# Performance work log

Measured on AMD Instinct MI355X. Metric: run time of the kernel, lower is better.

The kernel has to match this reference:

```python
import jax, jax.numpy as jnp
import numpy as np

BATCH, SEQ, D_MODEL = 4, 4096, 2048
DSTATE, N_HEADS = 64, 16
D_INNER = DSTATE * N_HEADS  # 1024, must equal d_mamba


def setup_inputs() -> dict:
    key = jax.random.key(0)
    ks = jax.random.split(key, 6)
    x_norm = jax.random.normal(ks[0], (BATCH, SEQ, D_MODEL), jnp.float32)
    inv = 1.0 / np.sqrt(D_MODEL)
    Wx = jax.random.normal(ks[1], (D_INNER, D_MODEL), jnp.float32) * inv
    # dt_proj: weight std 0.001, bias -4.0 (as in module init)
    Wdt = jax.random.normal(ks[2], (D_INNER, D_MODEL), jnp.float32) * 0.001
    b_dt = jnp.full((D_INNER,), -4.0, jnp.float32)
    WB = jax.random.normal(ks[3], (DSTATE, D_MODEL), jnp.float32) * inv
    WC = jax.random.normal(ks[4], (DSTATE, D_MODEL), jnp.float32) * inv
    A_log = jnp.tile(jnp.log(jnp.arange(1, DSTATE + 1, dtype=jnp.float32))[None, :], (N_HEADS, 1))
    Dp = jnp.ones((D_INNER,), jnp.float32)
    Wout = jax.random.normal(ks[5], (D_INNER, D_INNER), jnp.float32) * (1.0 / np.sqrt(D_INNER))
    return {"x_norm": x_norm, "Wx": Wx, "Wdt": Wdt, "b_dt": b_dt,
            "WB": WB, "WC": WC, "A_log": A_log, "Dp": Dp, "Wout": Wout}


def reference(x_norm, Wx, Wdt, b_dt, WB, WC, A_log, Dp, Wout):
    # projections
    x_ssm = jnp.einsum("btd,id->bti", x_norm, Wx)                       # (B,T,D_inner)
    dt = jax.nn.softplus(jnp.einsum("btd,id->bti", x_norm, Wdt) + b_dt)
    dt = jnp.clip(dt, 1e-4, 0.5)
    Bm = jnp.einsum("btd,nd->btn", x_norm, WB)                          # (B,T,N)
    Cm = jnp.einsum("btd,nd->btn", x_norm, WC)
    Bm = Bm / jnp.maximum(jnp.linalg.norm(Bm, axis=-1, keepdims=True), 1.0)
    Cm = Cm / jnp.maximum(jnp.linalg.norm(Cm, axis=-1, keepdims=True), 1.0)
    # discretized diagonal SSM: h_t = dA_t * h_{t-1} + dt_t * B_t * x_t
    A_neg = -jnp.exp(A_log.reshape(-1))                                  # (D_inner,)
    dA = jnp.exp(dt * A_neg)                                             # (B,T,D_inner)
    B_exp = jnp.tile(Bm, (1, 1, N_HEADS))                                # repeat across heads
    C_exp = jnp.tile(Cm, (1, 1, N_HEADS))
    dBx = dt * B_exp * x_ssm

    def combine(c1, c2):
        a1, b1 = c1
        a2, b2 = c2
        return a2 * a1, a2 * b1 + b2

    _, h = jax.lax.associative_scan(combine, (dA, dBx), axis=1)          # (B,T,D_inner)
    y = C_exp * h + Dp * x_ssm
    return jnp.einsum("bti,oi->bto", y, Wout)
```

## Files before the change

### kernel.cpp

```cpp
#include <hip/hip_runtime.h>
#include <hip/hip_bf16.h>
#include <math.h>

#define BATCH  4
#define SEQ    4096
#define DMODEL 2048
#define DSTATE 64
#define DINNER 1024
#define MTOT   (BATCH*SEQ)
#define NPROJ  (DINNER+DINNER+DSTATE+DSTATE)
#define CH     128
#define NC     (SEQ/CH)

typedef __attribute__((ext_vector_type(8))) short bf16x8;
typedef __attribute__((ext_vector_type(4))) float f32x4;

__device__ __forceinline__ unsigned short f2bf(float v) {
    __hip_bfloat16 b = __float2bfloat16(v);
    unsigned short u; __builtin_memcpy(&u, &b, 2); return u;
}
__device__ __forceinline__ float bf2f(unsigned short u) {
    __hip_bfloat16 b; __builtin_memcpy(&b, &u, 2); return __bfloat162float(b);
}
__device__ __forceinline__ void split2(float v, unsigned short& h, unsigned short& l) {
    h = f2bf(v);
    l = f2bf(v - bf2f(h));
}

__global__ __launch_bounds__(256, 2)
void proj_gemm(const float* __restrict__ X,
               const unsigned short* __restrict__ Wh,
               const unsigned short* __restrict__ Wl,
               const float* __restrict__ b_dt,
               float* __restrict__ x_ssm, float* __restrict__ dt,
               float* __restrict__ Bm,    float* __restrict__ Cm)
{
    __shared__ unsigned short Ahs[128*32];
    __shared__ unsigned short Als[128*32];
    __shared__ unsigned short Bhs[128*32];
    __shared__ unsigned short Bls[128*32];

    const int tid  = threadIdx.x;
    const int lane = tid & 63;
    const int w    = tid >> 6;
    const int wr   = (w >> 1) * 64;
    const int wc   = (w & 1)  * 64;
    const int l15  = lane & 15;
    const int lg   = lane >> 4;
    const int nblk = blockIdx.x * 128;
    const int mblk = blockIdx.y * 128;

    f32x4 acc[4][4];
    #pragma unroll
    for (int m = 0; m < 4; ++m)
        #pragma unroll
        for (int n = 0; n < 4; ++n)
            acc[m][n] = (f32x4){0.f, 0.f, 0.f, 0.f};

    for (int k0 = 0; k0 < DMODEL; k0 += 32) {
        float4 av[4];
        #pragma unroll
        for (int r = 0; r < 4; ++r) {
            int s   = r * 256 + tid;
            int row = s >> 3, seg = s & 7;
            av[r] = *reinterpret_cast<const float4*>(
                &X[(size_t)(mblk + row) * DMODEL + k0 + seg * 4]);
        }
        __syncthreads();
        #pragma unroll
        for (int r = 0; r < 4; ++r) {
            int s   = r * 256 + tid;
            int row = s >> 3, seg = s & 7;
            unsigned short h0,h1,h2,h3,l0,l1,l2,l3;
            split2(av[r].x, h0, l0); split2(av[r].y, h1, l1);
            split2(av[r].z, h2, l2); split2(av[r].w, h3, l3);
            *reinterpret_cast<ushort4*>(&Ahs[row*32 + seg*4]) = make_ushort4(h0,h1,h2,h3);
            *reinterpret_cast<ushort4*>(&Als[row*32 + seg*4]) = make_ushort4(l0,l1,l2,l3);
        }
        #pragma unroll
        for (int r = 0; r < 2; ++r) {
            int s    = r * 256 + tid;
            int row  = s >> 2, kseg = s & 3;
            const unsigned short* srch = &Wh[(size_t)(nblk + row) * DMODEL + k0 + kseg * 8];
            const unsigned short* srcl = &Wl[(size_t)(nblk + row) * DMODEL + k0 + kseg * 8];
            unsigned short* dsth = &Bhs[(size_t)(r * 256 + w * 64) * 8];
            unsigned short* dstl = &Bls[(size_t)(r * 256 + w * 64) * 8];
            __builtin_amdgcn_global_load_lds(
                (const __attribute__((address_space(1))) void*)srch,
                (__attribute__((address_space(3))) void*)dsth, 16, 0, 0);
            __builtin_amdgcn_global_load_lds(
                (const __attribute__((address_space(1))) void*)srcl,
                (__attribute__((address_space(3))) void*)dstl, 16, 0, 0);
        }
        __syncthreads();

        bf16x8 af[4][2], bfr[4][2];
        #pragma unroll
        for (int m = 0; m < 4; ++m) {
            int row = wr + m * 16 + l15;
            af[m][0] = *reinterpret_cast<const bf16x8*>(&Ahs[row*32 + lg*8]);
            af[m][1] = *reinterpret_cast<const bf16x8*>(&Als[row*32 + lg*8]);
        }
        #pragma unroll
        for (int n = 0; n < 4; ++n) {
            int row = wc + n * 16 + l15;
            bfr[n][0] = *reinterpret_cast<const bf16x8*>(&Bhs[row*32 + lg*8]);
            bfr[n][1] = *reinterpret_cast<const bf16x8*>(&Bls[row*32 + lg*8]);
        }
        #pragma unroll
        for (int m = 0; m < 4; ++m)
            #pragma unroll
            for (int n = 0; n < 4; ++n) {
                acc[m][n] = __builtin_amdgcn_mfma_f32_16x16x32_bf16(af[m][0], bfr[n][0], acc[m][n], 0, 0, 0);
                acc[m][n] = __builtin_amdgcn_mfma_f32_16x16x32_bf16(af[m][0], bfr[n][1], acc[m][n], 0, 0, 0);
                acc[m][n] = __builtin_amdgcn_mfma_f32_16x16x32_bf16(af[m][1], bfr[n][0], acc[m][n], 0, 0, 0);
            }
    }

    #pragma unroll
    for (int m = 0; m < 4; ++m) {
        #pragma unroll
        for (int n = 0; n < 4; ++n) {
            #pragma unroll
            for (int q = 0; q < 4; ++q) {
                int gm = mblk + wr + m * 16 + lg * 4 + q;
                int gn = nblk + wc + n * 16 + l15;
                float v = acc[m][n][q];
                if (gn < 1024) {
                    x_ssm[(size_t)gm * DINNER + gn] = v;
                } else if (gn < 2048) {
                    float z  = v + b_dt[gn - 1024];
                    float sp = z > 15.f ? z : log1pf(expf(z));
                    dt[(size_t)gm * DINNER + (gn - 1024)] =
                        fminf(fmaxf(sp, 1e-4f), 0.5f);
                } else if (gn < 2112) {
                    Bm[(size_t)gm * DSTATE + (gn - 2048)] = v;
                } else {
                    Cm[(size_t)gm * DSTATE + (gn - 2112)] = v;
                }
            }
        }
    }
}

__global__ __launch_bounds__(256, 2)
void out_gemm(const unsigned short* __restrict__ Yh, const unsigned short* __restrict__ Yl,
              const unsigned short* __restrict__ Woh, const unsigned short* __restrict__ Wol,
              float* __restrict__ Out)
{
    __shared__ unsigned short Ahs[128*32];
    __shared__ unsigned short Als[128*32];
    __shared__ unsigned short Bhs[128*32];
    __shared__ unsigned short Bls[128*32];

    const int tid  = threadIdx.x;
    const int lane = tid & 63;
    const int w    = tid >> 6;
    const int wr   = (w >> 1) * 64;
    const int wc   = (w & 1)  * 64;
    const int l15  = lane & 15;
    const int lg   = lane >> 4;
    const int nblk = blockIdx.x * 128;
    const int mblk = blockIdx.y * 128;

    f32x4 acc[4][4];
    #pragma unroll
    for (int m = 0; m < 4; ++m)
        #pragma unroll
        for (int n = 0; n < 4; ++n)
            acc[m][n] = (f32x4){0.f, 0.f, 0.f, 0.f};

    for (int k0 = 0; k0 < DINNER; k0 += 32) {
        __syncthreads();
        #pragma unroll
        for (int r = 0; r < 2; ++r) {
            int s    = r * 256 + tid;
            int row  = s >> 2, kseg = s & 3;
            size_t aoff = (size_t)(mblk + row) * DINNER + k0 + kseg * 8;
            size_t boff = (size_t)(nblk + row) * DINNER + k0 + kseg * 8;
            unsigned short* dbase_a_h = &Ahs[(size_t)(r * 256 + w * 64) * 8];
            unsigned short* dbase_a_l = &Als[(size_t)(r * 256 + w * 64) * 8];
            unsigned short* dbase_b_h = &Bhs[(size_t)(r * 256 + w * 64) * 8];
            unsigned short* dbase_b_l = &Bls[(size_t)(r * 256 + w * 64) * 8];
            __builtin_amdgcn_global_load_lds(
                (const __attribute__((address_space(1))) void*)&Yh[aoff],
                (__attribute__((address_space(3))) void*)dbase_a_h, 16, 0, 0);
            __builtin_amdgcn_global_load_lds(
                (const __attribute__((address_space(1))) void*)&Yl[aoff],
                (__attribute__((address_space(3))) void*)dbase_a_l, 16, 0, 0);
            __builtin_amdgcn_global_load_lds(
                (const __attribute__((address_space(1))) void*)&Woh[boff],
                (__attribute__((address_space(3))) void*)dbase_b_h, 16, 0, 0);
            __builtin_amdgcn_global_load_lds(
                (const __attribute__((address_space(1))) void*)&Wol[boff],
                (__attribute__((address_space(3))) void*)dbase_b_l, 16, 0, 0);
        }
        __syncthreads();

        bf16x8 af[4][2], bfr[4][2];
        #pragma unroll
        for (int m = 0; m < 4; ++m) {
            int row = wr + m * 16 + l15;
            af[m][0] = *reinterpret_cast<const bf16x8*>(&Ahs[row*32 + lg*8]);
            af[m][1] = *reinterpret_cast<const bf16x8*>(&Als[row*32 + lg*8]);
        }
        #pragma unroll
        for (int n = 0; n < 4; ++n) {
            int row = wc + n * 16 + l15;
            bfr[n][0] = *reinterpret_cast<const bf16x8*>(&Bhs[row*32 + lg*8]);
            bfr[n][1] = *reinterpret_cast<const bf16x8*>(&Bls[row*32 + lg*8]);
        }
        #pragma unroll
        for (int m = 0; m < 4; ++m)
            #pragma unroll
            for (int n = 0; n < 4; ++n) {
                acc[m][n] = __builtin_amdgcn_mfma_f32_16x16x32_bf16(af[m][0], bfr[n][0], acc[m][n], 0, 0, 0);
                acc[m][n] = __builtin_amdgcn_mfma_f32_16x16x32_bf16(af[m][0], bfr[n][1], acc[m][n], 0, 0, 0);
                acc[m][n] = __builtin_amdgcn_mfma_f32_16x16x32_bf16(af[m][1], bfr[n][0], acc[m][n], 0, 0, 0);
            }
    }

    #pragma unroll
    for (int m = 0; m < 4; ++m) {
        #pragma unroll
        for (int n = 0; n < 4; ++n) {
            #pragma unroll
            for (int q = 0; q < 4; ++q) {
                size_t gm = mblk + wr + m * 16 + lg * 4 + q;
                int    gn = nblk + wc + n * 16 + l15;
                Out[gm * DINNER + gn] = acc[m][n][q];
            }
        }
    }
}

__global__ void split_f32(const float* __restrict__ src, unsigned short* __restrict__ h,
                          unsigned short* __restrict__ l, int n4)
{
    int stride = gridDim.x * blockDim.x;
    for (int i = blockIdx.x * blockDim.x + threadIdx.x; i < n4; i += stride) {
        float4 v = reinterpret_cast<const float4*>(src)[i];
        unsigned short h0,h1,h2,h3,l0,l1,l2,l3;
        split2(v.x, h0, l0); split2(v.y, h1, l1);
        split2(v.z, h2, l2); split2(v.w, h3, l3);
        reinterpret_cast<ushort4*>(h)[i] = make_ushort4(h0,h1,h2,h3);
        reinterpret_cast<ushort4*>(l)[i] = make_ushort4(l0,l1,l2,l3);
    }
}

__global__ void normalize_bc(float* __restrict__ Bm, float* __restrict__ Cm)
{
    int w    = (blockIdx.x * blockDim.x + threadIdx.x) >> 6;
    int lane = threadIdx.x & 63;
    int row  = w >> 1;
    float* M = (w & 1) ? Cm : Bm;
    float v = M[(size_t)row * DSTATE + lane];
    float s = v * v;
    #pragma unroll
    for (int off = 32; off; off >>= 1) s += __shfl_xor(s, off);
    float scale = 1.0f / fmaxf(sqrtf(s), 1.0f);
    M[(size_t)row * DSTATE + lane] = v * scale;
}

__global__ void scan_passA(const float* __restrict__ dt, const float* __restrict__ x_ssm,
                           const float* __restrict__ Bm, const float* __restrict__ A_log,
                           float* __restrict__ Asum, float* __restrict__ Psum)
{
    int bi = blockIdx.x;
    int ib = bi & 3;
    int c  = (bi >> 2) & (NC - 1);
    int b  = bi >> 7;
    int i  = ib * 256 + threadIdx.x;
    float aneg = -expf(A_log[i]);
    float Aacc = 1.0f, P = 0.0f;
    size_t rowbase = (size_t)b * SEQ + (size_t)c * CH;
    for (int t = 0; t < CH; ++t) {
        size_t off = (rowbase + t) * DINNER + i;
        float d  = dt[off];
        float x  = x_ssm[off];
        float Bv = Bm[(rowbase + t) * DSTATE + (i & 63)];
        float a  = expf(d * aneg);
        Aacc *= a;
        P = fmaf(a, P, d * Bv * x);
    }
    size_t so = ((size_t)b * NC + c) * DINNER + i;
    Asum[so] = Aacc; Psum[so] = P;
}

__global__ void scan_chunkprefix(const float* __restrict__ Asum,
                                 const float* __restrict__ Psum,
                                 float* __restrict__ H)
{
    int idx = blockIdx.x * blockDim.x + threadIdx.x;
    int b = idx >> 10, i = idx & 1023;
    float h = 0.0f;
    for (int c = 0; c < NC; ++c) {
        size_t so = ((size_t)b * NC + c) * DINNER + i;
        H[so] = h;
        h = fmaf(Asum[so], h, Psum[so]);
    }
}

__global__ void scan_passB(const float* __restrict__ dt, const float* __restrict__ x_ssm,
                           const float* __restrict__ Bm, const float* __restrict__ Cm,
                           const float* __restrict__ A_log, const float* __restrict__ Dp,
                           const float* __restrict__ H,
                           unsigned short* __restrict__ Yh, unsigned short* __restrict__ Yl)
{
    int bi = blockIdx.x;
    int ib = bi & 3;
    int c  = (bi >> 2) & (NC - 1);
    int b  = bi >> 7;
    int i  = ib * 256 + threadIdx.x;
    float aneg = -expf(A_log[i]);
    float Dpi  = Dp[i];
    size_t so = ((size_t)b * NC + c) * DINNER + i;
    float h = H[so];
    size_t rowbase = (size_t)b * SEQ + (size_t)c * CH;
    for (int t = 0; t < CH; ++t) {
        size_t off = (rowbase + t) * DINNER + i;
        float d  = dt[off];
        float x  = x_ssm[off];
        float Bv = Bm[(rowbase + t) * DSTATE + (i & 63)];
        float Cv = Cm[(rowbase + t) * DSTATE + (i & 63)];
        float a  = expf(d * aneg);
        h = fmaf(a, h, d * Bv * x);
        float y = Cv * h + Dpi * x;
        unsigned short yh, yl;
        split2(y, yh, yl);
        Yh[off] = yh; Yl[off] = yl;
    }
}

extern "C" void kernel_launch(void* const* d_in, const int* in_sizes, int n_in,
                              void* d_out, int out_size, void* d_ws, size_t ws_size,
                              hipStream_t stream)
{
    const float* x_norm = (const float*)d_in[0];
    const float* Wx     = (const float*)d_in[1];
    const float* Wdt    = (const float*)d_in[2];
    const float* b_dt   = (const float*)d_in[3];
    const float* WB     = (const float*)d_in[4];
    const float* WC     = (const float*)d_in[5];
    const float* A_log  = (const float*)d_in[6];
    const float* Dp     = (const float*)d_in[7];
    const float* Wout   = (const float*)d_in[8];
    float* out = (float*)d_out;

    const size_t MB = 1024 * 1024;
    char* ws = (char*)d_ws;
    float* x_ssm = (float*)(ws);
    float* dtbuf = (float*)(ws + 64*MB);
    float* Bm    = (float*)(ws + 128*MB);
    float* Cm    = (float*)(ws + 132*MB);
    float* Asum  = (float*)(ws + 136*MB);
    float* Psum  = (float*)(ws + 136*MB + 512*1024);
    float* Hbuf  = (float*)(ws + 137*MB);
    unsigned short* Wh  = (unsigned short*)(ws + 138*MB);
    unsigned short* Wl  = (unsigned short*)(ws + 147*MB);
    unsigned short* Woh = (unsigned short*)(ws + 156*MB);
    unsigned short* Wol = (unsigned short*)(ws + 158*MB);
    unsigned short* Yh  = (unsigned short*)(ws + 160*MB);
    unsigned short* Yl  = (unsigned short*)(ws + 192*MB);

    const size_t WXN = (size_t)DINNER * DMODEL;
    const size_t WBN = (size_t)DSTATE * DMODEL;

    split_f32<<<1024, 256, 0, stream>>>(Wx,  Wh,             Wl,             (int)(WXN/4));
    split_f32<<<1024, 256, 0, stream>>>(Wdt, Wh + WXN,       Wl + WXN,       (int)(WXN/4));
    split_f32<<<64,   256, 0, stream>>>(WB,  Wh + 2*WXN,     Wl + 2*WXN,     (int)(WBN/4));
    split_f32<<<64,   256, 0, stream>>>(WC,  Wh + 2*WXN+WBN, Wl + 2*WXN+WBN, (int)(WBN/4));
    split_f32<<<1024, 256, 0, stream>>>(Wout, Woh, Wol, (int)((size_t)DINNER*DINNER/4));

    proj_gemm<<<dim3(NPROJ/128, MTOT/128), 256, 0, stream>>>(
        x_norm, Wh, Wl, b_dt, x_ssm, dtbuf, Bm, Cm);
    normalize_bc<<<(MTOT*2)/4, 256, 0, stream>>>(Bm, Cm);
    scan_passA<<<BATCH*NC*(DINNER/256), 256, 0, stream>>>(
        dtbuf, x_ssm, Bm, A_log, Asum, Psum);
    scan_chunkprefix<<<(BATCH*DINNER)/256, 256, 0, stream>>>(Asum, Psum, Hbuf);
    scan_passB<<<BATCH*NC*(DINNER/256), 256, 0, stream>>>(
        dtbuf, x_ssm, Bm, Cm, A_log, Dp, Hbuf, Yh, Yl);
    out_gemm<<<dim3(DINNER/128, MTOT/128), 256, 0, stream>>>(
        Yh, Yl, Woh, Wol, out);
}
```

Baseline: 968.1 us.

## XOR-swizzle LDS tiles and remap workgroups across XCDs in both GEMMs

Applies an XOR swizzle to the 16-byte column segments of the shared-memory A and B tiles in both GEMMs. Both the register-staged writes and the global_load_lds source addresses are permuted so the fragment reads hit different LDS banks. Workgroup IDs are remapped so consecutive blocks are spread across the 8 XCDs, aiming for better L2 reuse. The dt bias load is also hoisted out of the per-element loop. The swizzle adds a little address arithmetic and depends on the grid size being divisible by 8.

```diff
diff --git a/kernel.cpp b/kernel.cpp
--- a/kernel.cpp
+++ b/kernel.cpp
@@ -27,6 +27,11 @@
     l = f2bf(v - bf2f(h));
 }
 
+__device__ __forceinline__ bf16x8 frag_ld(const unsigned short* buf, int row, int lg) {
+    int j = lg ^ ((row >> 1) & 3);
+    return *reinterpret_cast<const bf16x8*>(&buf[row * 32 + j * 8]);
+}
+
 __global__ __launch_bounds__(256, 2)
 void proj_gemm(const float* __restrict__ X,
                const unsigned short* __restrict__ Wh,
@@ -47,8 +52,12 @@
     const int wc   = (w & 1)  * 64;
     const int l15  = lane & 15;
     const int lg   = lane >> 4;
-    const int nblk = blockIdx.x * 128;
-    const int mblk = blockIdx.y * 128;
+
+    const int nwg   = gridDim.x * gridDim.y;
+    const int bid   = blockIdx.y * gridDim.x + blockIdx.x;
+    const int swz   = (bid & 7) * (nwg >> 3) + (bid >> 3);
+    const int nblk  = (swz % gridDim.x) * 128;
+    const int mblk  = (swz / gridDim.x) * 128;
 
     f32x4 acc[4][4];
     #pragma unroll
@@ -71,18 +80,20 @@
         for (int r = 0; r < 4; ++r) {
             int s   = r * 256 + tid;
             int row = s >> 3, seg = s & 7;
+            int off = row * 32 + (((seg >> 1) ^ ((row >> 1) & 3)) * 8) + (seg & 1) * 4;
             unsigned short h0,h1,h2,h3,l0,l1,l2,l3;
             split2(av[r].x, h0, l0); split2(av[r].y, h1, l1);
             split2(av[r].z, h2, l2); split2(av[r].w, h3, l3);
-            *reinterpret_cast<ushort4*>(&Ahs[row*32 + seg*4]) = make_ushort4(h0,h1,h2,h3);
-            *reinterpret_cast<ushort4*>(&Als[row*32 + seg*4]) = make_ushort4(l0,l1,l2,l3);
+            *reinterpret_cast<ushort4*>(&Ahs[off]) = make_ushort4(h0,h1,h2,h3);
+            *reinterpret_cast<ushort4*>(&Als[off]) = make_ushort4(l0,l1,l2,l3);
         }
         #pragma unroll
         for (int r = 0; r < 2; ++r) {
             int s    = r * 256 + tid;
-            int row  = s >> 2, kseg = s & 3;
-            const unsigned short* srch = &Wh[(size_t)(nblk + row) * DMODEL + k0 + kseg * 8];
-            const unsigned short* srcl = &Wl[(size_t)(nblk + row) * DMODEL + k0 + kseg * 8];
+            int row  = s >> 2, j = s & 3;
+            int js   = j ^ ((row >> 1) & 3);
+            const unsigned short* srch = &Wh[(size_t)(nblk + row) * DMODEL + k0 + js * 8];
+            const unsigned short* srcl = &Wl[(size_t)(nblk + row) * DMODEL + k0 + js * 8];
             unsigned short* dsth = &Bhs[(size_t)(r * 256 + w * 64) * 8];
             unsigned short* dstl = &Bls[(size_t)(r * 256 + w * 64) * 8];
             __builtin_amdgcn_global_load_lds(
@@ -98,14 +109,14 @@
         #pragma unroll
         for (int m = 0; m < 4; ++m) {
             int row = wr + m * 16 + l15;
-            af[m][0] = *reinterpret_cast<const bf16x8*>(&Ahs[row*32 + lg*8]);
-            af[m][1] = *reinterpret_cast<const bf16x8*>(&Als[row*32 + lg*8]);
+            af[m][0] = frag_ld(Ahs, row, lg);
+            af[m][1] = frag_ld(Als, row, lg);
         }
         #pragma unroll
         for (int n = 0; n < 4; ++n) {
             int row = wc + n * 16 + l15;
-            bfr[n][0] = *reinterpret_cast<const bf16x8*>(&Bhs[row*32 + lg*8]);
-            bfr[n][1] = *reinterpret_cast<const bf16x8*>(&Bls[row*32 + lg*8]);
+            bfr[n][0] = frag_ld(Bhs, row, lg);
+            bfr[n][1] = frag_ld(Bls, row, lg);
         }
         #pragma unroll
         for (int m = 0; m < 4; ++m)
@@ -121,15 +132,16 @@
     for (int m = 0; m < 4; ++m) {
         #pragma unroll
         for (int n = 0; n < 4; ++n) {
+            int gn = nblk + wc + n * 16 + l15;
+            float bv = (gn >= 1024 && gn < 2048) ? b_dt[gn - 1024] : 0.0f;
             #pragma unroll
             for (int q = 0; q < 4; ++q) {
                 int gm = mblk + wr + m * 16 + lg * 4 + q;
-                int gn = nblk + wc + n * 16 + l15;
                 float v = acc[m][n][q];
                 if (gn < 1024) {
                     x_ssm[(size_t)gm * DINNER + gn] = v;
                 } else if (gn < 2048) {
-                    float z  = v + b_dt[gn - 1024];
+                    float z  = v + bv;
                     float sp = z > 15.f ? z : log1pf(expf(z));
                     dt[(size_t)gm * DINNER + (gn - 1024)] =
                         fminf(fmaxf(sp, 1e-4f), 0.5f);
@@ -160,8 +172,12 @@
     const int wc   = (w & 1)  * 64;
     const int l15  = lane & 15;
     const int lg   = lane >> 4;
-    const int nblk = blockIdx.x * 128;
-    const int mblk = blockIdx.y * 128;
+
+    const int nwg   = gridDim.x * gridDim.y;
+    const int bid   = blockIdx.y * gridDim.x + blockIdx.x;
+    const int swz   = (bid & 7) * (nwg >> 3) + (bid >> 3);
+    const int nblk  = (swz % gridDim.x) * 128;
+    const int mblk  = (swz / gridDim.x) * 128;
 
     f32x4 acc[4][4];
     #pragma unroll
@@ -175,25 +191,26 @@
         #pragma unroll
         for (int r = 0; r < 2; ++r) {
             int s    = r * 256 + tid;
-            int row  = s >> 2, kseg = s & 3;
-            size_t aoff = (size_t)(mblk + row) * DINNER + k0 + kseg * 8;
-            size_t boff = (size_t)(nblk + row) * DINNER + k0 + kseg * 8;
-            unsigned short* dbase_a_h = &Ahs[(size_t)(r * 256 + w * 64) * 8];
-            unsigned short* dbase_a_l = &Als[(size_t)(r * 256 + w * 64) * 8];
-            unsigned short* dbase_b_h = &Bhs[(size_t)(r * 256 + w * 64) * 8];
-            unsigned short* dbase_b_l = &Bls[(size_t)(r * 256 + w * 64) * 8];
+            int row  = s >> 2, j = s & 3;
+            int js   = j ^ ((row >> 1) & 3);
+            size_t aoff = (size_t)(mblk + row) * DINNER + k0 + js * 8;
+            size_t boff = (size_t)(nblk + row) * DINNER + k0 + js * 8;
+            unsigned short* da_h = &Ahs[(size_t)(r * 256 + w * 64) * 8];
+            unsigned short* da_l = &Als[(size_t)(r * 256 + w * 64) * 8];
+            unsigned short* db_h = &Bhs[(size_t)(r * 256 + w * 64) * 8];
+            unsigned short* db_l = &Bls[(size_t)(r * 256 + w * 64) * 8];
             __builtin_amdgcn_global_load_lds(
                 (const __attribute__((address_space(1))) void*)&Yh[aoff],
-                (__attribute__((address_space(3))) void*)dbase_a_h, 16, 0, 0);
+                (__attribute__((address_space(3))) void*)da_h, 16, 0, 0);
             __builtin_amdgcn_global_load_lds(
                 (const __attribute__((address_space(1))) void*)&Yl[aoff],
-                (__attribute__((address_space(3))) void*)dbase_a_l, 16, 0, 0);
+                (__attribute__((address_space(3))) void*)da_l, 16, 0, 0);
             __builtin_amdgcn_global_load_lds(
                 (const __attribute__((address_space(1))) void*)&Woh[boff],
-                (__attribute__((address_space(3))) void*)dbase_b_h, 16, 0, 0);
+                (__attribute__((address_space(3))) void*)db_h, 16, 0, 0);
             __builtin_amdgcn_global_load_lds(
                 (const __attribute__((address_space(1))) void*)&Wol[boff],
-                (__attribute__((address_space(3))) void*)dbase_b_l, 16, 0, 0);
+                (__attribute__((address_space(3))) void*)db_l, 16, 0, 0);
         }
         __syncthreads();
 
@@ -201,14 +218,14 @@
         #pragma unroll
         for (int m = 0; m < 4; ++m) {
             int row = wr + m * 16 + l15;
-            af[m][0] = *reinterpret_cast<const bf16x8*>(&Ahs[row*32 + lg*8]);
-            af[m][1] = *reinterpret_cast<const bf16x8*>(&Als[row*32 + lg*8]);
+            af[m][0] = frag_ld(Ahs, row, lg);
+            af[m][1] = frag_ld(Als, row, lg);
         }
         #pragma unroll
         for (int n = 0; n < 4; ++n) {
             int row = wc + n * 16 + l15;
-            bfr[n][0] = *reinterpret_cast<const bf16x8*>(&Bhs[row*32 + lg*8]);
-            bfr[n][1] = *reinterpret_cast<const bf16x8*>(&Bls[row*32 + lg*8]);
+            bfr[n][0] = frag_ld(Bhs, row, lg);
+            bfr[n][1] = frag_ld(Bls, row, lg);
         }
         #pragma unroll
         for (int m = 0; m < 4; ++m)
```

Measured after the change: 899.6 us. 1.08x faster.
